# Kernel tuning notes

Hardware: AMD Instinct MI355X
Metric: run time of the kernel (lower is better)

Reference implementation:

```python
import jax, jax.numpy as jnp
import numpy as np

NUM_HEADS = 12


def setup_inputs() -> dict:
    key = jax.random.key(0)
    ks = jax.random.split(key, 9)
    B, T, C = 4, 2048, 768
    s = 1.0 / np.sqrt(C)
    return {
        "x": jax.random.normal(ks[0], (B, T, C), dtype=jnp.float32),
        "wq": jax.random.normal(ks[1], (C, C), dtype=jnp.float32) * s,
        "bq": jnp.zeros((C,), dtype=jnp.float32),
        "wk": jax.random.normal(ks[2], (C, C), dtype=jnp.float32) * s,
        "bk": jnp.zeros((C,), dtype=jnp.float32),
        "wv": jax.random.normal(ks[3], (C, C), dtype=jnp.float32) * s,
        "bv": jnp.zeros((C,), dtype=jnp.float32),
        "wo": jax.random.normal(ks[4], (C, C), dtype=jnp.float32) * s,
        "bo": jnp.zeros((C,), dtype=jnp.float32),
    }


def reference(x, wq, bq, wk, bk, wv, bv, wo, bo):
    B, T, C = x.shape
    H = NUM_HEADS
    D = C // H
    scale = D ** -0.5
    # projections: weights stored as [in, out] so y = x @ w + b
    q = (x @ wq + bq).reshape(B, T, H, D).transpose(0, 2, 1, 3)  # [B,H,T,D]
    k = (x @ wk + bk).reshape(B, T, H, D).transpose(0, 2, 1, 3)
    v = (x @ wv + bv).reshape(B, T, H, D).transpose(0, 2, 1, 3)
    scores = jnp.einsum("bhqd,bhkd->bhqk", q, k) * scale  # [B,H,T,T]
    probs = jax.nn.softmax(scores, axis=-1)
    out = jnp.einsum("bhqk,bhkd->bhqd", probs, v)  # [B,H,T,D]
    out = out.transpose(0, 2, 1, 3).reshape(B, T, C)
    return out @ wo + bo
```

## Files before the change

### kernel.cpp

```cpp
#include <hip/hip_runtime.h>
#include <math.h>

#define NB 4
#define T_SEQ 2048
#define C_DIM 768
#define NH 12
#define HD 64
#define M_TOK (NB * T_SEQ)
#define NE ((size_t)M_TOK * C_DIM)
#define WE ((size_t)C_DIM * C_DIM)
#define QSCALE 0.18033688011112042f

typedef short bf16x8 __attribute__((ext_vector_type(8)));
typedef float f32x4 __attribute__((ext_vector_type(4)));
typedef unsigned short u16x4 __attribute__((ext_vector_type(4)));
typedef unsigned short u16x8 __attribute__((ext_vector_type(8)));
typedef unsigned short ushort_t;

__device__ __forceinline__ unsigned short f2bf(float x) {
    unsigned u = __float_as_uint(x);
    u += 0x7FFFu + ((u >> 16) & 1u);
    return (unsigned short)(u >> 16);
}
__device__ __forceinline__ float bf2f(unsigned short h) {
    return __uint_as_float(((unsigned)h) << 16);
}
__device__ __forceinline__ int sw128(int row, int bytecol) {
    return row * 128 + (bytecol ^ ((row & 7) << 4));
}
__device__ __forceinline__ void gload16(const ushort_t* gp, ushort_t* lp) {
    __builtin_amdgcn_global_load_lds(
        (const __attribute__((address_space(1))) unsigned int*)(const void*)gp,
        (__attribute__((address_space(3))) unsigned int*)(void*)lp, 16, 0, 0);
}

__global__ __launch_bounds__(256) void prep(
    const float* __restrict__ X,
    const float* __restrict__ wq, const float* __restrict__ wk,
    const float* __restrict__ wv, const float* __restrict__ wo,
    ushort_t* __restrict__ XH, ushort_t* __restrict__ Wbase)
{
    __shared__ float T[64][65];
    const int tid = threadIdx.x;
    const int bid = blockIdx.x;

    if (bid < 3072) {
        const size_t i = ((size_t)bid * 256 + tid) * 8;
        const float4 f0 = *(const float4*)&X[i];
        const float4 f1 = *(const float4*)&X[i + 4];
        const float xs[8] = {f0.x, f0.y, f0.z, f0.w, f1.x, f1.y, f1.z, f1.w};
        u16x8 h;
        #pragma unroll
        for (int j = 0; j < 8; ++j) h[j] = f2bf(xs[j]);
        *(u16x8*)&XH[i] = h;
        return;
    }

    const int r_ = bid - 3072;
    const int z = r_ / 144;
    const int rem = r_ % 144;
    const int ti = rem / 12, nj = rem % 12;
    const float* W = (z == 0) ? wq : (z == 1) ? wk : (z == 2) ? wv : wo;
    ushort_t* TH = Wbase + (size_t)z * 2 * WE;
    ushort_t* TL = TH + WE;
    {
        const int r = tid >> 2, cq = (tid & 3) * 16;
        #pragma unroll
        for (int j = 0; j < 4; ++j) {
            const float4 f = *(const float4*)&W[(size_t)(ti * 64 + r) * C_DIM + nj * 64 + cq + j * 4];
            T[r][cq + j * 4 + 0] = f.x;
            T[r][cq + j * 4 + 1] = f.y;
            T[r][cq + j * 4 + 2] = f.z;
            T[r][cq + j * 4 + 3] = f.w;
        }
    }
    __syncthreads();
    {
        const int n = tid >> 2, kq = (tid & 3) * 16;
        u16x8 h0, h1, l0, l1;
        #pragma unroll
        for (int j = 0; j < 8; ++j) {
            float v = T[kq + j][n];
            unsigned short hh = f2bf(v);
            h0[j] = hh; l0[j] = f2bf(v - bf2f(hh));
            v = T[kq + 8 + j][n];
            hh = f2bf(v);
            h1[j] = hh; l1[j] = f2bf(v - bf2f(hh));
        }
        const size_t o = (size_t)(nj * 64 + n) * C_DIM + ti * 64 + kq;
        *(u16x8*)&TH[o] = h0; *(u16x8*)&TH[o + 8] = h1;
        *(u16x8*)&TL[o] = l0; *(u16x8*)&TL[o + 8] = l1;
    }
}

__global__ __launch_bounds__(256, 4) void gemm_qkv(
    const ushort_t* __restrict__ XH,
    const ushort_t* __restrict__ WQH, const ushort_t* __restrict__ WKH,
    const ushort_t* __restrict__ WVH,
    const float* __restrict__ bq, const float* __restrict__ bk,
    const float* __restrict__ bv,
    ushort_t* __restrict__ Qo, ushort_t* __restrict__ Ko, ushort_t* __restrict__ VTo)
{
    __shared__ ushort_t TA[2][128 * 32];
    __shared__ ushort_t TB[2][128 * 32];

    const int tid = threadIdx.x, lane = tid & 63, w = tid >> 6;
    const int l15 = lane & 15, g = lane >> 4;
    const int wr = w >> 1, wc = w & 1;

    int bid = (int)blockIdx.x;
    bid = (bid & 7) * 144 + (bid >> 3);
    const int bm = bid / 18, bn = bid % 18;
    const int wsel = bn / 6, bnw = bn % 6;

    const ushort_t* BH = (wsel == 0) ? WQH : (wsel == 1) ? WKH : WVH;
    const float* bias = (wsel == 0) ? bq : (wsel == 1) ? bk : bv;

    f32x4 acc[4][4];
    #pragma unroll
    for (int m = 0; m < 4; ++m)
        #pragma unroll
        for (int n = 0; n < 4; ++n) acc[m][n] = (f32x4){0.f, 0.f, 0.f, 0.f};

    auto stage = [&](int buf, int k0) {
        #pragma unroll
        for (int p = 0; p < 4; ++p) {
            const int cb = 256 * p + 64 * w;
            const int c  = cb + lane;
            const int row = (c & 511) >> 2;
            const int slot = (c & 3) ^ ((row >> 1) & 3);
            if (cb < 512)
                gload16(XH + ((size_t)bm * 128 + row) * C_DIM + k0 + slot * 8,
                        &TA[buf][(cb & 511) * 8]);
            else
                gload16(BH + ((size_t)bnw * 128 + row) * C_DIM + k0 + slot * 8,
                        &TB[buf][(cb & 511) * 8]);
        }
    };

    stage(0, 0);
    int cur = 0;
    if (wsel < 2) {
        for (int k0 = 0; k0 < C_DIM; k0 += 32) {
            __syncthreads();
            if (k0 + 32 < C_DIM) stage(cur ^ 1, k0 + 32);
            bf16x8 ah[4], bh_[4];
            #pragma unroll
            for (int m = 0; m < 4; ++m) {
                const int r = 64 * wr + 16 * m + l15;
                const int off = r * 64 + ((g ^ ((r >> 1) & 3)) << 4);
                ah[m] = *(const bf16x8*)((const char*)TA[cur] + off);
            }
            #pragma unroll
            for (int n = 0; n < 4; ++n) {
                const int r = 64 * wc + 16 * n + l15;
                const int off = r * 64 + ((g ^ ((r >> 1) & 3)) << 4);
                bh_[n] = *(const bf16x8*)((const char*)TB[cur] + off);
            }
            #pragma unroll
            for (int m = 0; m < 4; ++m)
                #pragma unroll
                for (int n = 0; n < 4; ++n)
                    acc[m][n] = __builtin_amdgcn_mfma_f32_16x16x32_bf16(bh_[n], ah[m], acc[m][n], 0, 0, 0);
            cur ^= 1;
        }
        const float oscale = (wsel == 0) ? QSCALE : 1.0f;
        ushort_t* OH = (wsel == 0) ? Qo : Ko;
        #pragma unroll
        for (int n = 0; n < 4; ++n) {
            const int colw0 = bnw * 128 + 64 * wc + 16 * n + 4 * g;
            const float4 bv4 = *(const float4*)&bias[colw0];
            const float bvr[4] = {bv4.x, bv4.y, bv4.z, bv4.w};
            const int h = colw0 >> 6, d0 = colw0 & 63;
            #pragma unroll
            for (int m = 0; m < 4; ++m) {
                const int t = bm * 128 + 64 * wr + 16 * m + l15;
                const int b = t >> 11, tt = t & (T_SEQ - 1);
                u16x4 ph;
                #pragma unroll
                for (int r = 0; r < 4; ++r)
                    ph[r] = f2bf((acc[m][n][r] + bvr[r]) * oscale);
                *(u16x4*)&OH[(((size_t)b * NH + h) * T_SEQ + tt) * HD + d0] = ph;
            }
        }
    } else {
        for (int k0 = 0; k0 < C_DIM; k0 += 32) {
            __syncthreads();
            if (k0 + 32 < C_DIM) stage(cur ^ 1, k0 + 32);
            bf16x8 ah[4], bh_[4];
            #pragma unroll
            for (int m = 0; m < 4; ++m) {
                const int r = 64 * wr + 16 * m + l15;
                const int off = r * 64 + ((g ^ ((r >> 1) & 3)) << 4);
                ah[m] = *(const bf16x8*)((const char*)TA[cur] + off);
            }
            #pragma unroll
            for (int n = 0; n < 4; ++n) {
                const int r = 64 * wc + 16 * n + l15;
                const int off = r * 64 + ((g ^ ((r >> 1) & 3)) << 4);
                bh_[n] = *(const bf16x8*)((const char*)TB[cur] + off);
            }
            #pragma unroll
            for (int m = 0; m < 4; ++m)
                #pragma unroll
                for (int n = 0; n < 4; ++n)
                    acc[m][n] = __builtin_amdgcn_mfma_f32_16x16x32_bf16(ah[m], bh_[n], acc[m][n], 0, 0, 0);
            cur ^= 1;
        }
        #pragma unroll
        for (int n = 0; n < 4; ++n) {
            const int colw = bnw * 128 + 64 * wc + 16 * n + l15;
            const float bv_ = bias[colw];
            const int h = colw >> 6, d = colw & 63;
            #pragma unroll
            for (int m = 0; m < 4; ++m) {
                const int row0 = bm * 128 + 64 * wr + 16 * m + 4 * g;
                u16x4 ph;
                #pragma unroll
                for (int r = 0; r < 4; ++r) ph[r] = f2bf(acc[m][n][r] + bv_);
                const int b = row0 >> 11, t0 = row0 & (T_SEQ - 1);
                *(u16x4*)&VTo[(((size_t)b * NH + h) * HD + d) * T_SEQ + t0] = ph;
            }
        }
    }
}

__global__ __launch_bounds__(256, 4) void gemm_out(
    const ushort_t* __restrict__ AB,
    const ushort_t* __restrict__ BH, const ushort_t* __restrict__ BL,
    const float* __restrict__ bias, float* __restrict__ OutF)
{
    __shared__ ushort_t TA[2][128 * 32];
    __shared__ ushort_t TB[2][2][64 * 32];

    const int tid = threadIdx.x, lane = tid & 63, w = tid >> 6;
    const int l15 = lane & 15, g = lane >> 4;
    const int wr = w >> 1, wc = w & 1;

    int bid = (int)blockIdx.x;
    bid = (bid & 7) * 96 + (bid >> 3);
    const int bm = bid / 12, bn = bid % 12;

    f32x4 acc[4][2];
    #pragma unroll
    for (int m = 0; m < 4; ++m)
        #pragma unroll
        for (int n = 0; n < 2; ++n) acc[m][n] = (f32x4){0.f, 0.f, 0.f, 0.f};

    auto stage = [&](int buf, int k0) {
        #pragma unroll
        for (int p = 0; p < 4; ++p) {
            const int c = w + 4 * p;
            if (c < 8) {
                const int row = c * 16 + (lane >> 2);
                const int slot = (lane & 3) ^ ((row >> 1) & 3);
                gload16(AB + ((size_t)bm * 128 + row) * C_DIM + k0 + slot * 8,
                        &TA[buf][c * 512]);
            } else {
                const int t_ = (c - 8) >> 2;
                const int cc = c & 3;
                const int row = cc * 16 + (lane >> 2);
                const int slot = (lane & 3) ^ ((row >> 1) & 3);
                const ushort_t* src = (t_ ? BL : BH) + ((size_t)bn * 64 + row) * C_DIM + k0 + slot * 8;
                gload16(src, &TB[buf][t_][cc * 512]);
            }
        }
    };

    stage(0, 0);
    int cur = 0;
    for (int k0 = 0; k0 < C_DIM; k0 += 32) {
        __syncthreads();
        if (k0 + 32 < C_DIM) stage(cur ^ 1, k0 + 32);

        bf16x8 a_[4], bh_[2], bl_[2];
        #pragma unroll
        for (int m = 0; m < 4; ++m) {
            const int r = 64 * wr + 16 * m + l15;
            const int off = r * 64 + ((g ^ ((r >> 1) & 3)) << 4);
            a_[m] = *(const bf16x8*)((const char*)TA[cur] + off);
        }
        #pragma unroll
        for (int n = 0; n < 2; ++n) {
            const int r = 32 * wc + 16 * n + l15;
            const int off = r * 64 + ((g ^ ((r >> 1) & 3)) << 4);
            bh_[n] = *(const bf16x8*)((const char*)TB[cur][0] + off);
            bl_[n] = *(const bf16x8*)((const char*)TB[cur][1] + off);
        }
        #pragma unroll
        for (int m = 0; m < 4; ++m)
            #pragma unroll
            for (int n = 0; n < 2; ++n) {
                acc[m][n] = __builtin_amdgcn_mfma_f32_16x16x32_bf16(a_[m], bh_[n], acc[m][n], 0, 0, 0);
                acc[m][n] = __builtin_amdgcn_mfma_f32_16x16x32_bf16(a_[m], bl_[n], acc[m][n], 0, 0, 0);
            }
        cur ^= 1;
    }

    #pragma unroll
    for (int n = 0; n < 2; ++n) {
        const int col = bn * 64 + 32 * wc + 16 * n + l15;
        const float bv = bias[col];
        #pragma unroll
        for (int m = 0; m < 4; ++m) {
            const int row0 = bm * 128 + 64 * wr + 16 * m + 4 * g;
            #pragma unroll
            for (int r = 0; r < 4; ++r)
                OutF[(size_t)(row0 + r) * C_DIM + col] = acc[m][n][r] + bv;
        }
    }
}

__global__ __launch_bounds__(256, 4) void attn_fuse7(
    const ushort_t* __restrict__ QB, const ushort_t* __restrict__ KB,
    const ushort_t* __restrict__ VTB, ushort_t* __restrict__ ABo)
{
    __shared__ ushort_t Ks[64 * 64];
    __shared__ ushort_t Vt[64 * 64];
    __shared__ ushort_t Pm[4][32 * 64];

    const int tid = threadIdx.x, lane = tid & 63, w = tid >> 6;
    const int l15 = lane & 15, g = lane >> 4;

    int bid = (int)blockIdx.x;
    bid = (bid & 7) * 96 + (bid >> 3);
    const int bh = bid >> 4, qt = bid & 15;
    const int b = bh / NH, h = bh % NH;

    bf16x8 qf0[2], qf1[2];
    #pragma unroll
    for (int kc = 0; kc < 2; ++kc) {
        const size_t base = ((size_t)bh * T_SEQ + qt * 128 + 32 * w + l15) * HD + kc * 32 + g * 8;
        qf0[kc] = *(const bf16x8*)&QB[base];
        qf1[kc] = *(const bf16x8*)&QB[base + (size_t)16 * HD];
    }

    bf16x8 onesf;
    #pragma unroll
    for (int j = 0; j < 8; ++j) onesf[j] = (short)0x3F80;

    f32x4 o0[4], o1[4];
    #pragma unroll
    for (int nd = 0; nd < 4; ++nd) {
        o0[nd] = (f32x4){0.f, 0.f, 0.f, 0.f};
        o1[nd] = (f32x4){0.f, 0.f, 0.f, 0.f};
    }
    f32x4 ol0 = (f32x4){0.f, 0.f, 0.f, 0.f};
    f32x4 ol1 = (f32x4){0.f, 0.f, 0.f, 0.f};

    const ushort_t* kb = KB + (size_t)bh * T_SEQ * HD;
    const ushort_t* vb = VTB + (size_t)bh * HD * T_SEQ;
    const int swz = (l15 & 7) << 4;

    const ushort_t *gK0, *gK1, *gV0, *gV1;
    {
        const int c0 = w * 64 + lane;
        const int r0 = c0 >> 3;
        const int cb0 = ((c0 & 7) * 16) ^ ((r0 & 7) << 4);
        gK0 = kb + (size_t)r0 * HD + (cb0 >> 1);
        gV0 = vb + (size_t)r0 * T_SEQ + (cb0 >> 1);
        const int c1 = c0 + 256;
        const int r1 = c1 >> 3;
        const int cb1 = ((c1 & 7) * 16) ^ ((r1 & 7) << 4);
        gK1 = kb + (size_t)r1 * HD + (cb1 >> 1);
        gV1 = vb + (size_t)r1 * T_SEQ + (cb1 >> 1);
    }
    ushort_t* dK0 = &Ks[w * 512];
    ushort_t* dK1 = &Ks[2048 + w * 512];
    ushort_t* dV0 = &Vt[w * 512];
    ushort_t* dV1 = &Vt[2048 + w * 512];

    for (int kt = 0; kt < T_SEQ; kt += 64) {
        __syncthreads();
        gload16(gK0, dK0); gK0 += (size_t)64 * HD;
        gload16(gK1, dK1); gK1 += (size_t)64 * HD;
        gload16(gV0, dV0); gV0 += 64;
        gload16(gV1, dV1); gV1 += 64;
        __syncthreads();

        f32x4 s0[4], s1[4];
        #pragma unroll
        for (int nb = 0; nb < 4; ++nb) {
            s0[nb] = (f32x4){0.f, 0.f, 0.f, 0.f};
            s1[nb] = (f32x4){0.f, 0.f, 0.f, 0.f};
        }
        __builtin_amdgcn_s_setprio(1);
        #pragma unroll
        for (int kc = 0; kc < 2; ++kc)
            #pragma unroll
            for (int nb = 0; nb < 4; ++nb) {
                const bf16x8 kf = *(const bf16x8*)((const char*)Ks + sw128(16 * nb + l15, kc * 64 + g * 16));
                s0[nb] = __builtin_amdgcn_mfma_f32_16x16x32_bf16(kf, qf0[kc], s0[nb], 0, 0, 0);
                s1[nb] = __builtin_amdgcn_mfma_f32_16x16x32_bf16(kf, qf1[kc], s1[nb], 0, 0, 0);
            }
        __builtin_amdgcn_s_setprio(0);

        #pragma unroll
        for (int nb = 0; nb < 4; ++nb) {
            const float a0 = __builtin_amdgcn_exp2f(s0[nb][0]);
            const float a1 = __builtin_amdgcn_exp2f(s0[nb][1]);
            const float a2 = __builtin_amdgcn_exp2f(s0[nb][2]);
            const float a3 = __builtin_amdgcn_exp2f(s0[nb][3]);
            const unsigned dwa0 = __builtin_amdgcn_perm(
                __float_as_uint(a1), __float_as_uint(a0), 0x07060302u);
            const unsigned dwa1 = __builtin_amdgcn_perm(
                __float_as_uint(a3), __float_as_uint(a2), 0x07060302u);
            *(uint2*)((char*)Pm[w] + l15 * 128 + ((32 * nb + 8 * g) ^ swz)) =
                make_uint2(dwa0, dwa1);

            const float b0 = __builtin_amdgcn_exp2f(s1[nb][0]);
            const float b1 = __builtin_amdgcn_exp2f(s1[nb][1]);
            const float b2 = __builtin_amdgcn_exp2f(s1[nb][2]);
            const float b3 = __builtin_amdgcn_exp2f(s1[nb][3]);
            const unsigned dwb0 = __builtin_amdgcn_perm(
                __float_as_uint(b1), __float_as_uint(b0), 0x07060302u);
            const unsigned dwb1 = __builtin_amdgcn_perm(
                __float_as_uint(b3), __float_as_uint(b2), 0x07060302u);
            *(uint2*)((char*)Pm[w] + (16 + l15) * 128 + ((32 * nb + 8 * g) ^ swz)) =
                make_uint2(dwb0, dwb1);
        }

        #pragma unroll
        for (int kc2 = 0; kc2 < 2; ++kc2) {
            const bf16x8 pb0 = *(const bf16x8*)((const char*)Pm[w] + l15 * 128 + ((kc2 * 64 + g * 16) ^ swz));
            const bf16x8 pb1 = *(const bf16x8*)((const char*)Pm[w] + (16 + l15) * 128 + ((kc2 * 64 + g * 16) ^ swz));
            __builtin_amdgcn_s_setprio(1);
            #pragma unroll
            for (int nd = 0; nd < 4; ++nd) {
                const bf16x8 vf = *(const bf16x8*)((const char*)Vt + sw128(16 * nd + l15, kc2 * 64 + g * 16));
                o0[nd] = __builtin_amdgcn_mfma_f32_16x16x32_bf16(vf, pb0, o0[nd], 0, 0, 0);
                o1[nd] = __builtin_amdgcn_mfma_f32_16x16x32_bf16(vf, pb1, o1[nd], 0, 0, 0);
            }
            ol0 = __builtin_amdgcn_mfma_f32_16x16x32_bf16(onesf, pb0, ol0, 0, 0, 0);
            ol1 = __builtin_amdgcn_mfma_f32_16x16x32_bf16(onesf, pb1, ol1, 0, 0, 0);
            __builtin_amdgcn_s_setprio(0);
        }
    }

    const float inv0 = 1.0f / ol0[0];
    const float inv1 = 1.0f / ol1[0];
    const int t0 = qt * 128 + 32 * w + l15;
    #pragma unroll
    for (int nd = 0; nd < 4; ++nd) {
        u16x4 h0_, h1_;
        #pragma unroll
        for (int r = 0; r < 4; ++r) {
            h0_[r] = f2bf(o0[nd][r] * inv0);
            h1_[r] = f2bf(o1[nd][r] * inv1);
        }
        const size_t col = h * HD + 16 * nd + 4 * g;
        *(u16x4*)&ABo[((size_t)b * T_SEQ + t0) * C_DIM + col] = h0_;
        *(u16x4*)&ABo[((size_t)b * T_SEQ + t0 + 16) * C_DIM + col] = h1_;
    }
}

extern "C" void kernel_launch(void* const* d_in, const int* in_sizes, int n_in,
                              void* d_out, int out_size, void* d_ws, size_t ws_size,
                              hipStream_t stream)
{
    const float* x  = (const float*)d_in[0];
    const float* wq = (const float*)d_in[1];
    const float* bq = (const float*)d_in[2];
    const float* wk = (const float*)d_in[3];
    const float* bk = (const float*)d_in[4];
    const float* wv = (const float*)d_in[5];
    const float* bv = (const float*)d_in[6];
    const float* wo = (const float*)d_in[7];
    const float* bo = (const float*)d_in[8];

    ushort_t* Wbase = (ushort_t*)d_ws;
    ushort_t* WQ_H = Wbase;
    ushort_t* WK_H = Wbase + 2 * WE;
    ushort_t* WV_H = Wbase + 4 * WE;
    ushort_t* WO_H = Wbase + 6 * WE;
    ushort_t* WO_L = WO_H + WE;
    ushort_t* X_H  = Wbase + 8 * WE;
    ushort_t* K_B  = X_H + 2 * NE;
    ushort_t* VT_B = K_B + NE;
    ushort_t* Q_B = (ushort_t*)d_out;
    ushort_t* A_B = X_H;

    const dim3 blk(256);

    prep<<<3648, blk, 0, stream>>>(x, wq, wk, wv, wo, X_H, Wbase);

    gemm_qkv<<<1152, blk, 0, stream>>>(X_H, WQ_H, WK_H, WV_H,
                                       bq, bk, bv, Q_B, K_B, VT_B);

    attn_fuse7<<<768, blk, 0, stream>>>(Q_B, K_B, VT_B, A_B);

    gemm_out<<<768, blk, 0, stream>>>(A_B, WO_H, WO_L, bo, (float*)d_out);
}
```

Baseline: 147.7 us.

## Double-buffer K/V tiles in attention to overlap loads with MFMA compute

The attention kernel now keeps two LDS buffers each for K and V^T. The next 64-key tile is prefetched into the alternate buffer while the current tile is used for QK^T, softmax and PV, which drops one barrier per iteration. This doubles the K/V LDS footprint, so the launch bound falls from 4 to 3 blocks per CU. With 768 blocks the grid still fits in one wave.

```diff
diff --git a/kernel.cpp b/kernel.cpp
--- a/kernel.cpp
+++ b/kernel.cpp
@@ -311,12 +311,12 @@
     }
 }
 
-__global__ __launch_bounds__(256, 4) void attn_fuse7(
+__global__ __launch_bounds__(256, 3) void attn_fuse8(
     const ushort_t* __restrict__ QB, const ushort_t* __restrict__ KB,
     const ushort_t* __restrict__ VTB, ushort_t* __restrict__ ABo)
 {
-    __shared__ ushort_t Ks[64 * 64];
-    __shared__ ushort_t Vt[64 * 64];
+    __shared__ ushort_t Ks[2][64 * 64];
+    __shared__ ushort_t Vt[2][64 * 64];
     __shared__ ushort_t Pm[4][32 * 64];
 
     const int tid = threadIdx.x, lane = tid & 63, w = tid >> 6;
@@ -365,18 +365,27 @@
         gK1 = kb + (size_t)r1 * HD + (cb1 >> 1);
         gV1 = vb + (size_t)r1 * T_SEQ + (cb1 >> 1);
     }
-    ushort_t* dK0 = &Ks[w * 512];
-    ushort_t* dK1 = &Ks[2048 + w * 512];
-    ushort_t* dV0 = &Vt[w * 512];
-    ushort_t* dV1 = &Vt[2048 + w * 512];
-
+    ushort_t* dK0 = &Ks[0][w * 512];
+    ushort_t* dK1 = &Ks[0][2048 + w * 512];
+    ushort_t* dV0 = &Vt[0][w * 512];
+    ushort_t* dV1 = &Vt[0][2048 + w * 512];
+
+    auto stage = [&](int buf) {
+        const int o = buf * 4096;
+        gload16(gK0, dK0 + o); gK0 += (size_t)64 * HD;
+        gload16(gK1, dK1 + o); gK1 += (size_t)64 * HD;
+        gload16(gV0, dV0 + o); gV0 += 64;
+        gload16(gV1, dV1 + o); gV1 += 64;
+    };
+
+    stage(0);
+    int cur = 0;
     for (int kt = 0; kt < T_SEQ; kt += 64) {
         __syncthreads();
-        gload16(gK0, dK0); gK0 += (size_t)64 * HD;
-        gload16(gK1, dK1); gK1 += (size_t)64 * HD;
-        gload16(gV0, dV0); gV0 += 64;
-        gload16(gV1, dV1); gV1 += 64;
-        __syncthreads();
+        if (kt + 64 < T_SEQ) stage(cur ^ 1);
+
+        const char* ksb = (const char*)Ks + cur * 8192;
+        const char* vtb = (const char*)Vt + cur * 8192;
 
         f32x4 s0[4], s1[4];
         #pragma unroll
@@ -389,7 +398,7 @@
         for (int kc = 0; kc < 2; ++kc)
             #pragma unroll
             for (int nb = 0; nb < 4; ++nb) {
-                const bf16x8 kf = *(const bf16x8*)((const char*)Ks + sw128(16 * nb + l15, kc * 64 + g * 16));
+                const bf16x8 kf = *(const bf16x8*)(ksb + sw128(16 * nb + l15, kc * 64 + g * 16));
                 s0[nb] = __builtin_amdgcn_mfma_f32_16x16x32_bf16(kf, qf0[kc], s0[nb], 0, 0, 0);
                 s1[nb] = __builtin_amdgcn_mfma_f32_16x16x32_bf16(kf, qf1[kc], s1[nb], 0, 0, 0);
             }
@@ -427,7 +436,7 @@
             __builtin_amdgcn_s_setprio(1);
             #pragma unroll
             for (int nd = 0; nd < 4; ++nd) {
-                const bf16x8 vf = *(const bf16x8*)((const char*)Vt + sw128(16 * nd + l15, kc2 * 64 + g * 16));
+                const bf16x8 vf = *(const bf16x8*)(vtb + sw128(16 * nd + l15, kc2 * 64 + g * 16));
                 o0[nd] = __builtin_amdgcn_mfma_f32_16x16x32_bf16(vf, pb0, o0[nd], 0, 0, 0);
                 o1[nd] = __builtin_amdgcn_mfma_f32_16x16x32_bf16(vf, pb1, o1[nd], 0, 0, 0);
             }
@@ -435,6 +444,7 @@
             ol1 = __builtin_amdgcn_mfma_f32_16x16x32_bf16(onesf, pb1, ol1, 0, 0, 0);
             __builtin_amdgcn_s_setprio(0);
         }
+        cur ^= 1;
     }
 
     const float inv0 = 1.0f / ol0[0];
@@ -487,7 +497,7 @@
     gemm_qkv<<<1152, blk, 0, stream>>>(X_H, WQ_H, WK_H, WV_H,
                                        bq, bk, bv, Q_B, K_B, VT_B);
 
-    attn_fuse7<<<768, blk, 0, stream>>>(Q_B, K_B, VT_B, A_B);
+    attn_fuse8<<<768, blk, 0, stream>>>(Q_B, K_B, VT_B, A_B);
 
     gemm_out<<<768, blk, 0, stream>>>(A_B, WO_H, WO_L, bo, (float*)d_out);
 }
```

After: 147.9 us. No clear change (+0.2%).

## Halve attention block size to 64 queries with 2 waves, skip unused low-weight writes

Applied to the files above, without the earlier changes.

The attention kernel now runs 128-thread blocks that each handle 64 query rows, doubling the grid to 1536 blocks. Each thread loads four K/V chunks per tile instead of two. The remapped block index keeps one (batch,head) per group of 32 query tiles. The MFMA priority window is widened to cover the whole PV loop. The prep kernel also stops writing low-part bf16 weights except for the output projection weight (z==3), which cuts write traffic. In exchange, K/V tiles are now reloaded by twice as many blocks, and there are fewer waves per block to hide latency.

```diff
diff --git a/kernel.cpp b/kernel.cpp
--- a/kernel.cpp
+++ b/kernel.cpp
@@ -89,7 +89,9 @@
         }
         const size_t o = (size_t)(nj * 64 + n) * C_DIM + ti * 64 + kq;
         *(u16x8*)&TH[o] = h0; *(u16x8*)&TH[o + 8] = h1;
-        *(u16x8*)&TL[o] = l0; *(u16x8*)&TL[o + 8] = l1;
+        if (z == 3) {
+            *(u16x8*)&TL[o] = l0; *(u16x8*)&TL[o + 8] = l1;
+        }
     }
 }
 
@@ -311,26 +313,26 @@
     }
 }
 
-__global__ __launch_bounds__(256, 4) void attn_fuse7(
+__global__ __launch_bounds__(128, 3) void attn_fuse10(
     const ushort_t* __restrict__ QB, const ushort_t* __restrict__ KB,
     const ushort_t* __restrict__ VTB, ushort_t* __restrict__ ABo)
 {
     __shared__ ushort_t Ks[64 * 64];
     __shared__ ushort_t Vt[64 * 64];
-    __shared__ ushort_t Pm[4][32 * 64];
+    __shared__ ushort_t Pm[2][32 * 64];
 
     const int tid = threadIdx.x, lane = tid & 63, w = tid >> 6;
     const int l15 = lane & 15, g = lane >> 4;
 
     int bid = (int)blockIdx.x;
-    bid = (bid & 7) * 96 + (bid >> 3);
-    const int bh = bid >> 4, qt = bid & 15;
+    bid = (bid & 7) * 192 + (bid >> 3);
+    const int bh = bid >> 5, qt = bid & 31;
     const int b = bh / NH, h = bh % NH;
 
     bf16x8 qf0[2], qf1[2];
     #pragma unroll
     for (int kc = 0; kc < 2; ++kc) {
-        const size_t base = ((size_t)bh * T_SEQ + qt * 128 + 32 * w + l15) * HD + kc * 32 + g * 8;
+        const size_t base = ((size_t)bh * T_SEQ + qt * 64 + 32 * w + l15) * HD + kc * 32 + g * 8;
         qf0[kc] = *(const bf16x8*)&QB[base];
         qf1[kc] = *(const bf16x8*)&QB[base + (size_t)16 * HD];
     }
@@ -352,30 +354,24 @@
     const ushort_t* vb = VTB + (size_t)bh * HD * T_SEQ;
     const int swz = (l15 & 7) << 4;
 
-    const ushort_t *gK0, *gK1, *gV0, *gV1;
-    {
-        const int c0 = w * 64 + lane;
-        const int r0 = c0 >> 3;
-        const int cb0 = ((c0 & 7) * 16) ^ ((r0 & 7) << 4);
-        gK0 = kb + (size_t)r0 * HD + (cb0 >> 1);
-        gV0 = vb + (size_t)r0 * T_SEQ + (cb0 >> 1);
-        const int c1 = c0 + 256;
-        const int r1 = c1 >> 3;
-        const int cb1 = ((c1 & 7) * 16) ^ ((r1 & 7) << 4);
-        gK1 = kb + (size_t)r1 * HD + (cb1 >> 1);
-        gV1 = vb + (size_t)r1 * T_SEQ + (cb1 >> 1);
-    }
-    ushort_t* dK0 = &Ks[w * 512];
-    ushort_t* dK1 = &Ks[2048 + w * 512];
-    ushort_t* dV0 = &Vt[w * 512];
-    ushort_t* dV1 = &Vt[2048 + w * 512];
+    const ushort_t *gK[4], *gV[4];
+    #pragma unroll
+    for (int i = 0; i < 4; ++i) {
+        const int c = 64 * w + lane + 128 * i;
+        const int row = c >> 3;
+        const int colb = ((c & 7) * 16) ^ ((row & 7) << 4);
+        gK[i] = kb + (size_t)row * HD + (colb >> 1);
+        gV[i] = vb + (size_t)row * T_SEQ + (colb >> 1);
+    }
 
     for (int kt = 0; kt < T_SEQ; kt += 64) {
         __syncthreads();
-        gload16(gK0, dK0); gK0 += (size_t)64 * HD;
-        gload16(gK1, dK1); gK1 += (size_t)64 * HD;
-        gload16(gV0, dV0); gV0 += 64;
-        gload16(gV1, dV1); gV1 += 64;
+        #pragma unroll
+        for (int i = 0; i < 4; ++i) {
+            const int cb = 64 * w + 128 * i;
+            gload16(gK[i], &Ks[cb * 8]); gK[i] += (size_t)64 * HD;
+            gload16(gV[i], &Vt[cb * 8]); gV[i] += 64;
+        }
         __syncthreads();
 
         f32x4 s0[4], s1[4];
@@ -420,11 +416,11 @@
                 make_uint2(dwb0, dwb1);
         }
 
+        __builtin_amdgcn_s_setprio(1);
         #pragma unroll
         for (int kc2 = 0; kc2 < 2; ++kc2) {
             const bf16x8 pb0 = *(const bf16x8*)((const char*)Pm[w] + l15 * 128 + ((kc2 * 64 + g * 16) ^ swz));
             const bf16x8 pb1 = *(const bf16x8*)((const char*)Pm[w] + (16 + l15) * 128 + ((kc2 * 64 + g * 16) ^ swz));
-            __builtin_amdgcn_s_setprio(1);
             #pragma unroll
             for (int nd = 0; nd < 4; ++nd) {
                 const bf16x8 vf = *(const bf16x8*)((const char*)Vt + sw128(16 * nd + l15, kc2 * 64 + g * 16));
@@ -433,13 +429,13 @@
             }
             ol0 = __builtin_amdgcn_mfma_f32_16x16x32_bf16(onesf, pb0, ol0, 0, 0, 0);
             ol1 = __builtin_amdgcn_mfma_f32_16x16x32_bf16(onesf, pb1, ol1, 0, 0, 0);
-            __builtin_amdgcn_s_setprio(0);
-        }
+        }
+        __builtin_amdgcn_s_setprio(0);
     }
 
     const float inv0 = 1.0f / ol0[0];
     const float inv1 = 1.0f / ol1[0];
-    const int t0 = qt * 128 + 32 * w + l15;
+    const int t0 = qt * 64 + 32 * w + l15;
     #pragma unroll
     for (int nd = 0; nd < 4; ++nd) {
         u16x4 h0_, h1_;
@@ -487,7 +483,7 @@
     gemm_qkv<<<1152, blk, 0, stream>>>(X_H, WQ_H, WK_H, WV_H,
                                        bq, bk, bv, Q_B, K_B, VT_B);
 
-    attn_fuse7<<<768, blk, 0, stream>>>(Q_B, K_B, VT_B, A_B);
+    attn_fuse10<<<1536, dim3(128), 0, stream>>>(Q_B, K_B, VT_B, A_B);
 
     gemm_out<<<768, blk, 0, stream>>>(A_B, WO_H, WO_L, bo, (float*)d_out);
 }
```

Result: slower. 155.5 us (+5.3%).
